# Kernel optimization log

Hardware: AMD Instinct MI355X
Metric: run time of the kernel (lower is better)

Reference implementation:

```python
import jax, jax.numpy as jnp
import numpy as np

N = 50000
E = 800000
IN_CH = 128
OUT_CH = 32
HEADS = 2
NEG_SLOPE = 0.2


def setup_inputs() -> dict:
    key = jax.random.key(0)
    k_x, k_ei, k_w, k_as, k_ad, k_b = jax.random.split(key, 6)
    x = jax.random.normal(k_x, (N, IN_CH), dtype=jnp.float32)
    edge_index = jax.random.randint(k_ei, (2, E), 0, N, dtype=jnp.int64)
    # Glorot-style init scale for linear weight and attention vectors
    w_scale = 1.0 / np.sqrt(IN_CH)
    W = jax.random.normal(k_w, (IN_CH, HEADS * OUT_CH), dtype=jnp.float32) * w_scale
    a_scale = 1.0 / np.sqrt(OUT_CH)
    a_src = jax.random.normal(k_as, (HEADS, OUT_CH), dtype=jnp.float32) * a_scale
    a_dst = jax.random.normal(k_ad, (HEADS, OUT_CH), dtype=jnp.float32) * a_scale
    bias = jnp.zeros((HEADS * OUT_CH,), dtype=jnp.float32)
    return {"x": x, "edge_index": edge_index, "W": W, "a_src": a_src,
            "a_dst": a_dst, "bias": bias}


def reference(x, edge_index, W, a_src, a_dst, bias):
    n = x.shape[0]
    # add self-loops (add_self_loops=True); static shape E+N
    loops = jnp.tile(jnp.arange(n, dtype=edge_index.dtype), (2, 1))
    ei = jnp.concatenate([edge_index, loops], axis=1)
    src, dst = ei[0], ei[1]

    # linear projection -> per-head features [N, H, C]
    h = (x @ W).reshape(n, HEADS, OUT_CH)

    # per-node attention logits [N, H]
    alpha_s = jnp.sum(h * a_src[None], axis=-1)
    alpha_d = jnp.sum(h * a_dst[None], axis=-1)

    # per-edge score, LeakyReLU, segment softmax over edges grouped by dst
    e = jax.nn.leaky_relu(alpha_s[src] + alpha_d[dst], NEG_SLOPE)  # [E', H]
    e_max = jax.ops.segment_max(e, dst, num_segments=n)           # [N, H]
    e_exp = jnp.exp(e - e_max[dst])
    denom = jax.ops.segment_sum(e_exp, dst, num_segments=n)       # [N, H]
    alpha = e_exp / (denom[dst] + 1e-16)                          # [E', H]

    # scatter-add weighted messages [N, H, C]
    out = jax.ops.segment_sum(alpha[:, :, None] * h[src], dst, num_segments=n)
    # concat heads + bias (concat=True)
    return out.reshape(n, HEADS * OUT_CH) + bias
```

## Files before the change

### kernel.cpp

```cpp
#include <hip/hip_runtime.h>
#include <hip/hip_bf16.h>
#include <hip/hip_fp16.h>
#include <math.h>

#define IN_CH   128
#define OUT_CH  32
#define HEADS   2
#define HC      (HEADS * OUT_CH)
#define NEG_SLOPE 0.2f

#define NODE_TILE 64
#define LDS_STRIDE 136

#define BIN_CAP 64

typedef _Float16 h2_t __attribute__((ext_vector_type(2)));
union V16 { int4 v; h2_t h[4]; };

__device__ __forceinline__ float fdot2(h2_t a, h2_t b, float c) {
#if __has_builtin(__builtin_amdgcn_fdot2)
    return __builtin_amdgcn_fdot2(a, b, c, false);
#else
    return c + (float)a.x * (float)b.x + (float)a.y * (float)b.y;
#endif
}

__global__ __launch_bounds__(256) void gemm_hist_kernel(
    const float* __restrict__ x, const float* __restrict__ W,
    const float* __restrict__ a_src, const float* __restrict__ a_dst,
    __half* __restrict__ h, float* __restrict__ alpha_s, float* __restrict__ alpha_d,
    const int* __restrict__ dst, int* __restrict__ deg, int* __restrict__ rank,
    int n_nodes, int n_edges, int n_total, int gemm_blocks)
{
    const int tid = threadIdx.x;

    if (blockIdx.x >= gemm_blocks) {
        int e = (blockIdx.x - gemm_blocks) * blockDim.x + tid;
        if (e < n_total) {
            int d = (e < n_edges) ? dst[e] : (e - n_edges);
            rank[e] = atomicAdd(&deg[d], 1);
        }
        return;
    }

    __shared__ _Float16 Wt[HC * LDS_STRIDE];
    __shared__ _Float16 Xs[NODE_TILE * LDS_STRIDE];

    const int node0 = blockIdx.x * NODE_TILE;

    const float4* W4 = (const float4*)W;
    #pragma unroll
    for (int i = 0; i < 8; ++i) {
        int idx4 = tid + i * 256;
        int k  = idx4 >> 4;
        int c4 = idx4 & 15;
        float4 v = W4[idx4];
        Wt[(c4 * 4 + 0) * LDS_STRIDE + k] = (_Float16)v.x;
        Wt[(c4 * 4 + 1) * LDS_STRIDE + k] = (_Float16)v.y;
        Wt[(c4 * 4 + 2) * LDS_STRIDE + k] = (_Float16)v.z;
        Wt[(c4 * 4 + 3) * LDS_STRIDE + k] = (_Float16)v.w;
    }

    const float4* X4 = (const float4*)x;
    #pragma unroll
    for (int i = 0; i < 8; ++i) {
        int idx4 = tid + i * 256;
        int r = idx4 >> 5, c4 = idx4 & 31;
        int node = node0 + r;
        float4 v = make_float4(0.f, 0.f, 0.f, 0.f);
        if (node < n_nodes) v = X4[(size_t)node * (IN_CH / 4) + c4];
        _Float16 hv[4] = {(_Float16)v.x, (_Float16)v.y, (_Float16)v.z, (_Float16)v.w};
        *(int2*)&Xs[r * LDS_STRIDE + c4 * 4] = *(int2*)hv;
    }
    __syncthreads();

    const int n    = tid >> 3;
    const int g    = tid & 7;
    const int col0 = g * 8;
    const int head = col0 >> 5;
    const int c0   = col0 & 31;

    float accA[8] = {0,0,0,0,0,0,0,0};
    float accB[8] = {0,0,0,0,0,0,0,0};
    const _Float16* xa = &Xs[n * LDS_STRIDE];
    const _Float16* xb = &Xs[(n + 32) * LDS_STRIDE];

    for (int k0 = 0; k0 < IN_CH; k0 += 8) {
        V16 va, vb;
        va.v = *(const int4*)&xa[k0];
        vb.v = *(const int4*)&xb[k0];
        #pragma unroll
        for (int j = 0; j < 8; ++j) {
            V16 w;
            w.v = *(const int4*)&Wt[(col0 + j) * LDS_STRIDE + k0];
            float a = accA[j], b = accB[j];
            a = fdot2(w.h[0], va.h[0], a); b = fdot2(w.h[0], vb.h[0], b);
            a = fdot2(w.h[1], va.h[1], a); b = fdot2(w.h[1], vb.h[1], b);
            a = fdot2(w.h[2], va.h[2], a); b = fdot2(w.h[2], vb.h[2], b);
            a = fdot2(w.h[3], va.h[3], a); b = fdot2(w.h[3], vb.h[3], b);
            accA[j] = a; accB[j] = b;
        }
    }

    float asr[8], adr[8];
    #pragma unroll
    for (int j = 0; j < 8; ++j) {
        asr[j] = a_src[head * OUT_CH + c0 + j];
        adr[j] = a_dst[head * OUT_CH + c0 + j];
    }

    #pragma unroll
    for (int half = 0; half < 2; ++half) {
        const float* acc = half ? accB : accA;
        const int node = node0 + n + half * 32;
        if (node < n_nodes) {
            unsigned u[8];
            #pragma unroll
            for (int j = 0; j < 8; ++j) u[j] = __half_as_ushort(__float2half_rn(acc[j]));
            int4 v = make_int4((int)(u[0] | (u[1] << 16)), (int)(u[2] | (u[3] << 16)),
                               (int)(u[4] | (u[5] << 16)), (int)(u[6] | (u[7] << 16)));
            *(int4*)&h[(size_t)node * HC + col0] = v;
        }
        float ps = 0.f, pd = 0.f;
        #pragma unroll
        for (int j = 0; j < 8; ++j) { ps += acc[j] * asr[j]; pd += acc[j] * adr[j]; }
        ps += __shfl_xor(ps, 1); ps += __shfl_xor(ps, 2);
        pd += __shfl_xor(pd, 1); pd += __shfl_xor(pd, 2);
        if ((g & 3) == 0 && node < n_nodes) {
            alpha_s[node * HEADS + head] = ps;
            alpha_d[node * HEADS + head] = pd;
        }
    }
}

__global__ void fill_kernel(const int* __restrict__ src, const int* __restrict__ dst,
                            const int* __restrict__ rank,
                            const float* __restrict__ alpha_s, const float* __restrict__ alpha_d,
                            int2* __restrict__ bins, int n_edges, int n_total)
{
    int e = blockIdx.x * blockDim.x + threadIdx.x;
    if (e >= n_total) return;
    int s, d;
    if (e < n_edges) { s = src[e]; d = dst[e]; }
    else             { s = d = e - n_edges; }
    float2 as = ((const float2*)alpha_s)[s];
    float2 ad = ((const float2*)alpha_d)[d];
    int rk = rank[e];
    float v0 = as.x + ad.x;
    float v1 = as.y + ad.y;
    v0 = (v0 > 0.f) ? v0 : NEG_SLOPE * v0;
    v1 = (v1 > 0.f) ? v1 : NEG_SLOPE * v1;
    unsigned u0 = __half_as_ushort(__float2half_rn(__expf(v0)));
    unsigned u1 = __half_as_ushort(__float2half_rn(__expf(v1)));
    if (rk < BIN_CAP) {
        int2 rec;
        rec.x = s;
        rec.y = (int)((u1 << 16) | u0);
        bins[(size_t)d * BIN_CAP + rk] = rec;
    }
}

__device__ __forceinline__ float unpack_p(int py, int head) {
    unsigned u = (unsigned)py;
    unsigned short us = (unsigned short)(head ? (u >> 16) : (u & 0xffffu));
    return __half2float(__ushort_as_half(us));
}

__global__ __launch_bounds__(256) void node_gather_kernel(
    const int2* __restrict__ bins, const int* __restrict__ deg,
    const __half* __restrict__ h, const float* __restrict__ bias,
    float* __restrict__ out, int n_nodes)
{
    int node = blockIdx.x * (blockDim.x >> 6) + (threadIdx.x >> 6);
    if (node >= n_nodes) return;
    const int lane = threadIdx.x & 63;
    const int head = lane >> 5;
    int cnt = deg[node];
    if (cnt > BIN_CAP) cnt = BIN_CAP;
    const int2* ep = bins + (size_t)node * BIN_CAP;

    int rx = 0, ry = 0;
    if (lane < cnt) { int2 r = ep[lane]; rx = r.x; ry = r.y; }

    float acc = 0.f, lsum = 0.f;
    for (int i = 0; i < cnt; i += 16) {
        #pragma unroll
        for (int j = 0; j < 16; ++j) {
            int idx = i + j;
            int sj = __shfl(rx, idx);
            int yj = __shfl(ry, idx);
            float pj = (idx < cnt) ? unpack_p(yj, head) : 0.f;
            float hj = __half2float(h[(size_t)sj * HC + lane]);
            acc += pj * hj;
            lsum += pj;
        }
    }
    out[(size_t)node * HC + lane] = acc / (lsum + 1e-16f) + bias[lane];
}

extern "C" void kernel_launch(void* const* d_in, const int* in_sizes, int n_in,
                              void* d_out, int out_size, void* d_ws, size_t ws_size,
                              hipStream_t stream)
{
    const float* x      = (const float*)d_in[0];
    const int*   ei     = (const int*)d_in[1];
    const float* W      = (const float*)d_in[2];
    const float* a_src  = (const float*)d_in[3];
    const float* a_dst  = (const float*)d_in[4];
    const float* bias   = (const float*)d_in[5];
    float* out = (float*)d_out;

    const int n_nodes = in_sizes[0] / IN_CH;
    const int n_edges = in_sizes[1] / 2;
    const int n_total = n_edges + n_nodes;

    const int* src = ei;
    const int* dst = ei + n_edges;

    __half* h      = (__half*)d_ws;
    float* alpha_s = (float*)(h + (size_t)n_nodes * HC);
    float* alpha_d = alpha_s + (size_t)n_nodes * HEADS;
    int* deg       = (int*)(alpha_d + (size_t)n_nodes * HEADS);
    int* rank      = deg + n_nodes;
    uintptr_t ep   = (uintptr_t)(rank + n_total);
    ep = (ep + 15) & ~(uintptr_t)15;
    int2* bins     = (int2*)ep;

    const int edge_blocks = (n_total + 255) / 256;
    const int gemm_blocks = (n_nodes + NODE_TILE - 1) / NODE_TILE;

    hipMemsetAsync(deg, 0, (size_t)n_nodes * sizeof(int), stream);

    gemm_hist_kernel<<<gemm_blocks + edge_blocks, 256, 0, stream>>>(
        x, W, a_src, a_dst, h, alpha_s, alpha_d,
        dst, deg, rank, n_nodes, n_edges, n_total, gemm_blocks);

    fill_kernel<<<edge_blocks, 256, 0, stream>>>(
        src, dst, rank, alpha_s, alpha_d, bins, n_edges, n_total);

    int ng_blocks = (n_nodes + 3) / 4;
    node_gather_kernel<<<ng_blocks, 256, 0, stream>>>(
        bins, deg, h, bias, out, n_nodes);
}
```

Before: 163.9 us.

## Drop fill kernel: scatter src ids at histogram time, compute scores in gather

The histogram pass now writes the source index straight into the per-destination bin slot returned by its atomic, which removes the rank array and the separate fill kernel. The gather kernel then loads alpha_s per neighbour and recomputes LeakyReLU and exp itself, instead of reading precomputed fp16 weights. Bins shrink from int2 to int, and one launch and one pass over the edges go away. In exchange, each gather step adds a dependent load and an exp, and the odd redundant src loads in the histogram branch (dst[e - n_edges] used as src) look confusing but do address the src half of edge_index.

```diff
diff --git a/kernel.cpp b/kernel.cpp
--- a/kernel.cpp
+++ b/kernel.cpp
@@ -29,7 +29,7 @@
     const float* __restrict__ x, const float* __restrict__ W,
     const float* __restrict__ a_src, const float* __restrict__ a_dst,
     __half* __restrict__ h, float* __restrict__ alpha_s, float* __restrict__ alpha_d,
-    const int* __restrict__ dst, int* __restrict__ deg, int* __restrict__ rank,
+    const int* __restrict__ dst, int* __restrict__ deg, int* __restrict__ bins4,
     int n_nodes, int n_edges, int n_total, int gemm_blocks)
 {
     const int tid = threadIdx.x;
@@ -37,8 +37,13 @@
     if (blockIdx.x >= gemm_blocks) {
         int e = (blockIdx.x - gemm_blocks) * blockDim.x + tid;
         if (e < n_total) {
-            int d = (e < n_edges) ? dst[e] : (e - n_edges);
-            rank[e] = atomicAdd(&deg[d], 1);
+            int s, d;
+            if (e < n_edges) { s = __ldg(&dst[e - n_edges + n_edges]);  }
+            if (e < n_edges) { s = 0; }
+            if (e < n_edges) { d = dst[e]; s = dst[e - n_edges]; }
+            else             { s = d = e - n_edges; }
+            int rk = atomicAdd(&deg[d], 1);
+            if (rk < BIN_CAP) bins4[(size_t)d * BIN_CAP + rk] = s;
         }
         return;
     }
@@ -133,41 +138,9 @@
     }
 }
 
-__global__ void fill_kernel(const int* __restrict__ src, const int* __restrict__ dst,
-                            const int* __restrict__ rank,
-                            const float* __restrict__ alpha_s, const float* __restrict__ alpha_d,
-                            int2* __restrict__ bins, int n_edges, int n_total)
-{
-    int e = blockIdx.x * blockDim.x + threadIdx.x;
-    if (e >= n_total) return;
-    int s, d;
-    if (e < n_edges) { s = src[e]; d = dst[e]; }
-    else             { s = d = e - n_edges; }
-    float2 as = ((const float2*)alpha_s)[s];
-    float2 ad = ((const float2*)alpha_d)[d];
-    int rk = rank[e];
-    float v0 = as.x + ad.x;
-    float v1 = as.y + ad.y;
-    v0 = (v0 > 0.f) ? v0 : NEG_SLOPE * v0;
-    v1 = (v1 > 0.f) ? v1 : NEG_SLOPE * v1;
-    unsigned u0 = __half_as_ushort(__float2half_rn(__expf(v0)));
-    unsigned u1 = __half_as_ushort(__float2half_rn(__expf(v1)));
-    if (rk < BIN_CAP) {
-        int2 rec;
-        rec.x = s;
-        rec.y = (int)((u1 << 16) | u0);
-        bins[(size_t)d * BIN_CAP + rk] = rec;
-    }
-}
-
-__device__ __forceinline__ float unpack_p(int py, int head) {
-    unsigned u = (unsigned)py;
-    unsigned short us = (unsigned short)(head ? (u >> 16) : (u & 0xffffu));
-    return __half2float(__ushort_as_half(us));
-}
-
 __global__ __launch_bounds__(256) void node_gather_kernel(
-    const int2* __restrict__ bins, const int* __restrict__ deg,
+    const int* __restrict__ bins4, const int* __restrict__ deg,
+    const float* __restrict__ alpha_s, const float* __restrict__ alpha_d,
     const __half* __restrict__ h, const float* __restrict__ bias,
     float* __restrict__ out, int n_nodes)
 {
@@ -177,20 +150,26 @@
     const int head = lane >> 5;
     int cnt = deg[node];
     if (cnt > BIN_CAP) cnt = BIN_CAP;
-    const int2* ep = bins + (size_t)node * BIN_CAP;
-
-    int rx = 0, ry = 0;
-    if (lane < cnt) { int2 r = ep[lane]; rx = r.x; ry = r.y; }
+    const int* brow = bins4 + (size_t)node * BIN_CAP;
+    const float2* as2 = (const float2*)alpha_s;
+
+    float2 adn = ((const float2*)alpha_d)[node];
+    const float adv = head ? adn.y : adn.x;
+
+    int sreg = 0;
+    if (lane < cnt) sreg = brow[lane];
 
     float acc = 0.f, lsum = 0.f;
     for (int i = 0; i < cnt; i += 16) {
         #pragma unroll
         for (int j = 0; j < 16; ++j) {
             int idx = i + j;
-            int sj = __shfl(rx, idx);
-            int yj = __shfl(ry, idx);
-            float pj = (idx < cnt) ? unpack_p(yj, head) : 0.f;
+            int sj = __shfl(sreg, idx);
+            float2 a2 = as2[sj];
             float hj = __half2float(h[(size_t)sj * HC + lane]);
+            float v = (head ? a2.y : a2.x) + adv;
+            v = (v > 0.f) ? v : NEG_SLOPE * v;
+            float pj = (idx < cnt) ? __expf(v) : 0.f;
             acc += pj * hj;
             lsum += pj;
         }
@@ -214,17 +193,13 @@
     const int n_edges = in_sizes[1] / 2;
     const int n_total = n_edges + n_nodes;
 
-    const int* src = ei;
     const int* dst = ei + n_edges;
 
     __half* h      = (__half*)d_ws;
     float* alpha_s = (float*)(h + (size_t)n_nodes * HC);
     float* alpha_d = alpha_s + (size_t)n_nodes * HEADS;
     int* deg       = (int*)(alpha_d + (size_t)n_nodes * HEADS);
-    int* rank      = deg + n_nodes;
-    uintptr_t ep   = (uintptr_t)(rank + n_total);
-    ep = (ep + 15) & ~(uintptr_t)15;
-    int2* bins     = (int2*)ep;
+    int* bins4     = deg + n_nodes;
 
     const int edge_blocks = (n_total + 255) / 256;
     const int gemm_blocks = (n_nodes + NODE_TILE - 1) / NODE_TILE;
@@ -233,12 +208,9 @@
 
     gemm_hist_kernel<<<gemm_blocks + edge_blocks, 256, 0, stream>>>(
         x, W, a_src, a_dst, h, alpha_s, alpha_d,
-        dst, deg, rank, n_nodes, n_edges, n_total, gemm_blocks);
-
-    fill_kernel<<<edge_blocks, 256, 0, stream>>>(
-        src, dst, rank, alpha_s, alpha_d, bins, n_edges, n_total);
+        dst, deg, bins4, n_nodes, n_edges, n_total, gemm_blocks);
 
     int ng_blocks = (n_nodes + 3) / 4;
     node_gather_kernel<<<ng_blocks, 256, 0, stream>>>(
-        bins, deg, h, bias, out, n_nodes);
-}
+        bins4, deg, alpha_s, alpha_d, h, bias, out, n_nodes);
+}
```

Measured after the change: 205.1 us. 1.25x slower.
